# Kernel tuning notes

Measured on AMD Instinct MI355X. Metric: run time of the kernel, lower is better.

The kernel has to match this reference:

```python
import jax, jax.numpy as jnp
import numpy as np

N_NODES = 150000
N_EDGES = 300000
N_GRAPHS = 6000
HID = 256


def _lin_init(key, fan_in, fan_out):
    k1, k2 = jax.random.split(key)
    s = 1.0 / np.sqrt(fan_in)
    W = jax.random.uniform(k1, (fan_in, fan_out), jnp.float32, -s, s)
    b = jax.random.uniform(k2, (fan_out,), jnp.float32, -s, s)
    return W, b


def setup_inputs() -> dict:
    key = jax.random.key(0)
    ks = jax.random.split(key, 16)
    x = jax.random.normal(ks[0], (N_NODES, 7), jnp.float32)
    edge_index = jax.random.randint(ks[1], (2, N_EDGES), 0, N_NODES, jnp.int64)
    batch = jnp.sort(jax.random.randint(ks[2], (N_NODES,), 0, N_GRAPHS, jnp.int64))
    inp = {"x": x, "edge_index": edge_index, "batch": batch}
    dims_in = [7, HID, HID, HID]
    for i in range(4):
        Wa, ba = _lin_init(ks[3 + 2 * i], dims_in[i], HID)
        Wb, bb = _lin_init(ks[4 + 2 * i], HID, HID)
        inp[f"W{i+1}a"], inp[f"b{i+1}a"] = Wa, ba
        inp[f"W{i+1}b"], inp[f"b{i+1}b"] = Wb, bb
    inp["Wh1"], inp["bh1"] = _lin_init(ks[11], HID, 128)
    inp["Wh2"], inp["bh2"] = _lin_init(ks[12], 128, 3)
    return inp


def _gin_layer(x, src, dst, Wa, ba, Wb, bb):
    # sum-aggregate neighbor features: messages from src scattered to dst
    agg = jax.ops.segment_sum(x[src], dst, num_segments=N_NODES)
    h = agg + x  # (1 + eps) * x with eps = 0
    h = jax.nn.relu(h @ Wa + ba) @ Wb + bb  # GIN MLP
    return jax.nn.relu(h)  # outer F.relu in forward


def reference(x, edge_index, batch,
              W1a, b1a, W1b, b1b,
              W2a, b2a, W2b, b2b,
              W3a, b3a, W3b, b3b,
              W4a, b4a, W4b, b4b,
              Wh1, bh1, Wh2, bh2):
    src, dst = edge_index[0], edge_index[1]
    h = _gin_layer(x, src, dst, W1a, b1a, W1b, b1b)
    h = _gin_layer(h, src, dst, W2a, b2a, W2b, b2b)
    h = _gin_layer(h, src, dst, W3a, b3a, W3b, b3b)
    h = _gin_layer(h, src, dst, W4a, b4a, W4b, b4b)
    # global mean pool per graph
    sums = jax.ops.segment_sum(h, batch, num_segments=N_GRAPHS)
    counts = jax.ops.segment_sum(jnp.ones((N_NODES,), h.dtype), batch, num_segments=N_GRAPHS)
    pooled = sums / jnp.maximum(counts, 1.0)[:, None]
    # head (Dropout is identity in eval mode)
    out = jax.nn.relu(pooled @ Wh1 + bh1) @ Wh2 + bh2
    return out
```

## Files before the change

kernel.cpp:

```cpp
#include <hip/hip_runtime.h>

using bf16x8 = __attribute__((ext_vector_type(8))) __bf16;
using bf16x4 = __attribute__((ext_vector_type(4))) __bf16;
using f32x4  = __attribute__((ext_vector_type(4))) float;

#define MN    150000
#define NEDGE 300000
#define NG    6000
#define NSCAN 586

__device__ __forceinline__ float loadF(const void* p, size_t i, int f32) {
    return f32 ? ((const float*)p)[i] : (float)((const __bf16*)p)[i];
}
__device__ __forceinline__ int loadI(const int* p, size_t i, int i64) {
    return i64 ? p[2 * i] : p[i];
}

__global__ void k_probe(const void* W1a, const int* ei, const int* batch, int* flags) {
    __shared__ int s_f32, s_einz, s_bnz;
    if (threadIdx.x == 0) { s_f32 = 0; s_einz = 0; s_bnz = 0; }
    __syncthreads();
    const unsigned short* w = (const unsigned short*)W1a;
    for (int i = threadIdx.x; i < 1792; i += 256) {
        int e = (w[i] >> 7) & 0xFF;
        if (e >= 0xF0) s_f32 = 1;
    }
    for (int i = threadIdx.x; i < 2048; i += 256)
        if (ei[2 * i + 1] != 0) s_einz = 1;
    for (int i = threadIdx.x; i < 2048; i += 256)
        if (batch[75000 + 2 * i + 1] != 0) s_bnz = 1;
    __syncthreads();
    if (threadIdx.x == 0) {
        flags[0] = s_f32;
        flags[1] = s_einz ? 0 : 1;
        flags[2] = s_bnz ? 0 : 1;
    }
}

__global__ void k_zero_i32(int* p, int n) {
    int i = blockIdx.x * 256 + threadIdx.x;
    if (i < n) p[i] = 0;
}
__global__ void k_zero_f32(float* p, int n) {
    int i = blockIdx.x * 256 + threadIdx.x;
    if (i < n) p[i] = 0.f;
}

__global__ void k_cvtWT(const void* W0, const void* W1, const void* W2, const void* W3,
                        const void* W4, const void* W5, const void* W6,
                        __bf16* __restrict__ Wt, const int* __restrict__ flags) {
    int j = blockIdx.x >> 8;
    int n = blockIdx.x & 255, k = threadIdx.x;
    const void* Ws[7] = {W0, W1, W2, W3, W4, W5, W6};
    Wt[(size_t)j * 65536 + (size_t)n * 256 + k] = (__bf16)loadF(Ws[j], (size_t)k * 256 + n, flags[0]);
}

__global__ void k_deg(const int* __restrict__ ei, int* __restrict__ cnt, int nE,
                      const int* __restrict__ flags) {
    int e = blockIdx.x * 256 + threadIdx.x;
    if (e >= nE) return;
    int i64 = flags[1];
    int d = loadI(ei, (size_t)nE + e, i64);
    if ((unsigned)d >= (unsigned)MN) d = 0;
    atomicAdd(&cnt[d], 1);
}
__global__ void k_blksum(const int* __restrict__ cnt, int* __restrict__ bsum, int n) {
    __shared__ int s[256];
    int t = threadIdx.x;
    int i = blockIdx.x * 256 + t;
    s[t] = (i < n) ? cnt[i] : 0;
    __syncthreads();
    for (int o = 128; o > 0; o >>= 1) {
        if (t < o) s[t] += s[t + o];
        __syncthreads();
    }
    if (t == 0) bsum[blockIdx.x] = s[0];
}
__global__ __launch_bounds__(1024) void k_scanb(const int* __restrict__ bsum,
                                                int* __restrict__ bbase, int nb) {
    __shared__ int s[1024];
    int t = threadIdx.x;
    int v = (t < nb) ? bsum[t] : 0;
    s[t] = v;
    __syncthreads();
#pragma unroll
    for (int o = 1; o < 1024; o <<= 1) {
        int x = (t >= o) ? s[t - o] : 0;
        __syncthreads();
        s[t] += x;
        __syncthreads();
    }
    if (t < nb) bbase[t] = s[t] - v;
}
__global__ void k_blkscan(const int* __restrict__ cnt, const int* __restrict__ bbase,
                          int* __restrict__ offs, int n) {
    __shared__ int s[256];
    int t = threadIdx.x;
    int i = blockIdx.x * 256 + t;
    int v = (i < n) ? cnt[i] : 0;
    s[t] = v;
    __syncthreads();
    for (int o = 1; o < 256; o <<= 1) {
        int x = (t >= o) ? s[t - o] : 0;
        __syncthreads();
        s[t] += x;
        __syncthreads();
    }
    if (i < n) offs[i] = bbase[blockIdx.x] + s[t] - v;
}
__global__ void k_fill(const int* __restrict__ ei, const int* __restrict__ offs,
                       int* __restrict__ cur, int* __restrict__ elist, int nE,
                       const int* __restrict__ flags) {
    int e = blockIdx.x * 256 + threadIdx.x;
    if (e >= nE) return;
    int i64 = flags[1];
    int s = loadI(ei, (size_t)e, i64);
    int d = loadI(ei, (size_t)nE + e, i64);
    if ((unsigned)s >= (unsigned)MN) s = 0;
    if ((unsigned)d >= (unsigned)MN) d = 0;
    int pos = offs[d] + atomicAdd(&cur[d], 1);
    if ((unsigned)pos < (unsigned)NEDGE) elist[pos] = s;
}

__global__ __launch_bounds__(256) void k_l1lite(
    const void* __restrict__ x, const int* __restrict__ offs,
    const int* __restrict__ deg, const int* __restrict__ elist,
    float* __restrict__ agg7, const int* __restrict__ flags, int M_) {
    int f32 = flags[0];
    int t = threadIdx.x;
    int v = blockIdx.x * 32 + (t >> 3);
    int j = t & 7;
    if (v >= M_ || j >= 7) return;
    float s = loadF(x, (size_t)v * 7 + j, f32);
    int b = offs[v], d = min(deg[v], 1024);
    for (int e = 0; e < d; ++e) {
        int u = elist[b + e];
        if ((unsigned)u >= (unsigned)MN) u = 0;
        s += loadF(x, (size_t)u * 7 + j, f32);
    }
    agg7[(size_t)v * 8 + j] = s;
}

template<int CI, int MI>
__device__ __forceinline__ void gemm_core(const __bf16* lA, const __bf16* __restrict__ WT,
                                          int n0, int lm, int lq, f32x4 acc[CI][MI]) {
    const __bf16* wp = WT + (size_t)(n0 + lm) * 256 + lq * 8;
    bf16x8 wf[CI], wn[CI];
#pragma unroll
    for (int ci = 0; ci < CI; ++ci)
        wf[ci] = *(const bf16x8*)(wp + ci * 16 * 256);
#pragma unroll
    for (int kt = 0; kt < 8; ++kt) {
        if (kt < 7) {
#pragma unroll
            for (int ci = 0; ci < CI; ++ci)
                wn[ci] = *(const bf16x8*)(wp + ci * 16 * 256 + (kt + 1) * 32);
        }
        int sw = (((kt * 4 + lq) ^ (lm & 7)) << 3);
        bf16x8 xf[MI];
#pragma unroll
        for (int mi = 0; mi < MI; ++mi)
            xf[mi] = *(const bf16x8*)(lA + (mi * 16 + lm) * 256 + sw);
#pragma unroll
        for (int ci = 0; ci < CI; ++ci)
#pragma unroll
            for (int mi = 0; mi < MI; ++mi)
                acc[ci][mi] = __builtin_amdgcn_mfma_f32_16x16x32_bf16(
                    wf[ci], xf[mi], acc[ci][mi], 0, 0, 0);
#pragma unroll
        for (int ci = 0; ci < CI; ++ci) wf[ci] = wn[ci];
    }
}

template<int CI, int MI>
__device__ __forceinline__ void epi_to_lds(__bf16* lA, f32x4 acc[CI][MI], const void* bias,
                                           int n0, int lm, int lq, int f32) {
#pragma unroll
    for (int ci = 0; ci < CI; ++ci) {
        int n4 = n0 + ci * 16 + lq * 4;
        float b0 = loadF(bias, n4 + 0, f32), b1 = loadF(bias, n4 + 1, f32);
        float b2 = loadF(bias, n4 + 2, f32), b3 = loadF(bias, n4 + 3, f32);
#pragma unroll
        for (int mi = 0; mi < MI; ++mi) {
            int m = mi * 16 + lm;
            f32x4 a = acc[ci][mi];
            bf16x4 v;
            v[0] = (__bf16)fmaxf(a[0] + b0, 0.f);
            v[1] = (__bf16)fmaxf(a[1] + b1, 0.f);
            v[2] = (__bf16)fmaxf(a[2] + b2, 0.f);
            v[3] = (__bf16)fmaxf(a[3] + b3, 0.f);
            *(bf16x4*)(lA + m * 256 + (((n4 >> 3) ^ (m & 7)) << 3) + (n4 & 7)) = v;
        }
    }
}

template<int RW>
__device__ __forceinline__ void lds_to_global(const __bf16* lA, __bf16* __restrict__ Y,
                                              int bm, int w, int lane, int M_) {
    int half = lane >> 5;
    int cc = lane & 31;
#pragma unroll
    for (int it = 0; it < RW / 2; ++it) {
        int r = w * RW + it * 2 + half;
        int gm = bm + r;
        if (gm < M_) {
            bf16x8 v = *(const bf16x8*)(lA + r * 256 + ((cc ^ (r & 7)) << 3));
            *(bf16x8*)(Y + (size_t)gm * 256 + cc * 8) = v;
        }
    }
}

__device__ __forceinline__ void stage128_agg512(const __bf16* __restrict__ H, __bf16* lA,
                                                const int* __restrict__ offs,
                                                const int* __restrict__ deg,
                                                const int* __restrict__ elist,
                                                int bm, int t, int M_) {
    int tc = t & 7;
    int rl = t >> 3;
#pragma unroll 1
    for (int p = 0; p < 2; ++p) {
        int r = p * 64 + rl;
        int gr = bm + r;
        if (gr >= M_) gr = M_ - 1;
        const __bf16* self = H + (size_t)gr * 256 + tc * 32;
        float acc[32];
        {
            bf16x8 v0 = *(const bf16x8*)(self + 0);
            bf16x8 v1 = *(const bf16x8*)(self + 8);
            bf16x8 v2 = *(const bf16x8*)(self + 16);
            bf16x8 v3 = *(const bf16x8*)(self + 24);
#pragma unroll
            for (int j = 0; j < 8; ++j) {
                acc[j]      = (float)v0[j];
                acc[8 + j]  = (float)v1[j];
                acc[16 + j] = (float)v2[j];
                acc[24 + j] = (float)v3[j];
            }
        }
        int b = offs[gr], d = min(deg[gr], 1024);
        int e = 0;
        for (; e + 1 < d; e += 2) {
            int u0 = elist[b + e];
            int u1 = elist[b + e + 1];
            if ((unsigned)u0 >= (unsigned)MN) u0 = 0;
            if ((unsigned)u1 >= (unsigned)MN) u1 = 0;
            const __bf16* nb0 = H + (size_t)u0 * 256 + tc * 32;
            const __bf16* nb1 = H + (size_t)u1 * 256 + tc * 32;
            bf16x8 a0 = *(const bf16x8*)(nb0 + 0);
            bf16x8 a1 = *(const bf16x8*)(nb0 + 8);
            bf16x8 a2 = *(const bf16x8*)(nb0 + 16);
            bf16x8 a3 = *(const bf16x8*)(nb0 + 24);
            bf16x8 c0 = *(const bf16x8*)(nb1 + 0);
            bf16x8 c1 = *(const bf16x8*)(nb1 + 8);
            bf16x8 c2 = *(const bf16x8*)(nb1 + 16);
            bf16x8 c3 = *(const bf16x8*)(nb1 + 24);
#pragma unroll
            for (int j = 0; j < 8; ++j) {
                acc[j]      += (float)a0[j] + (float)c0[j];
                acc[8 + j]  += (float)a1[j] + (float)c1[j];
                acc[16 + j] += (float)a2[j] + (float)c2[j];
                acc[24 + j] += (float)a3[j] + (float)c3[j];
            }
        }
        if (e < d) {
            int u = elist[b + e];
            if ((unsigned)u >= (unsigned)MN) u = 0;
            const __bf16* nb = H + (size_t)u * 256 + tc * 32;
            bf16x8 n0 = *(const bf16x8*)(nb + 0);
            bf16x8 n1 = *(const bf16x8*)(nb + 8);
            bf16x8 n2 = *(const bf16x8*)(nb + 16);
            bf16x8 n3 = *(const bf16x8*)(nb + 24);
#pragma unroll
            for (int j = 0; j < 8; ++j) {
                acc[j]      += (float)n0[j];
                acc[8 + j]  += (float)n1[j];
                acc[16 + j] += (float)n2[j];
                acc[24 + j] += (float)n3[j];
            }
        }
#pragma unroll
        for (int q = 0; q < 4; ++q) {
            int c = tc * 4 + q;
            bf16x8 o;
#pragma unroll
            for (int j = 0; j < 8; ++j) o[j] = (__bf16)acc[q * 8 + j];
            *(bf16x8*)(lA + r * 256 + ((c ^ (r & 7)) << 3)) = o;
        }
    }
}

__global__ __launch_bounds__(512, 4) void k_agg_mlp(
    const __bf16* __restrict__ H, const int* __restrict__ offs, const int* __restrict__ deg,
    const int* __restrict__ elist,
    const __bf16* __restrict__ WaT, const void* __restrict__ ba,
    const __bf16* __restrict__ WbT, const void* __restrict__ bb,
    __bf16* __restrict__ Y, const int* __restrict__ batch,
    float* __restrict__ pool, float* __restrict__ cntf, int do_pool,
    int M_, const int* __restrict__ flags) {
    __shared__ __align__(16) __bf16 lA[128 * 256];
    __shared__ int sbatch[128];
    int t = threadIdx.x;
    int f32 = flags[0];
    int bm = blockIdx.x * 128;
    int w = t >> 6, lane = t & 63, lm = lane & 15, lq = lane >> 4;
    int n0 = w * 32;

    stage128_agg512(H, lA, offs, deg, elist, bm, t, M_);
    if (do_pool && t < 128) {
        int gm = bm + t;
        sbatch[t] = (gm < M_) ? loadI(batch, gm, flags[2]) : -1;
    }
    __syncthreads();

    {
        f32x4 acc[2][8] = {};
        gemm_core<2, 8>(lA, WaT, n0, lm, lq, acc);
        __syncthreads();
        epi_to_lds<2, 8>(lA, acc, ba, n0, lm, lq, f32);
    }
    __syncthreads();

    f32x4 acc2[2][8] = {};
    gemm_core<2, 8>(lA, WbT, n0, lm, lq, acc2);
    __syncthreads();
    epi_to_lds<2, 8>(lA, acc2, bb, n0, lm, lq, f32);
    __syncthreads();

    if (!do_pool) {
        lds_to_global<16>(lA, Y, bm, w, lane, M_);
    } else {
        int c = t & 255;
        int h2 = t >> 8;
        int g = -1;
        float acc = 0.f, run = 0.f;
        int rbeg = h2 * 64;
        for (int r = rbeg; r < rbeg + 64; ++r) {
            int bg = sbatch[r];
            if (bg < 0) break;
            if ((unsigned)bg >= (unsigned)NG) bg = 0;
            float v = (float)lA[r * 256 + (((c >> 3) ^ (r & 7)) << 3) + (c & 7)];
            if (bg != g) {
                if (g >= 0) {
                    atomicAdd(&pool[(size_t)g * 256 + c], acc);
                    if (c == 0) atomicAdd(&cntf[g], run);
                }
                g = bg; acc = 0.f; run = 0.f;
            }
            acc += v; run += 1.f;
        }
        if (g >= 0) {
            atomicAdd(&pool[(size_t)g * 256 + c], acc);
            if (c == 0) atomicAdd(&cntf[g], run);
        }
    }
}

__global__ __launch_bounds__(256, 2) void k_gemm1(
    const float* __restrict__ agg7, const void* __restrict__ W1a, const void* __restrict__ b1a,
    const __bf16* __restrict__ WT, const void* __restrict__ bias,
    __bf16* __restrict__ Y, int M_, const int* __restrict__ flags) {
    __shared__ __align__(16) __bf16 lA[128 * 256];
    __shared__ float sW[7 * 256];
    __shared__ float sB[256];
    int t = threadIdx.x;
    int f32 = flags[0];
    int bm = blockIdx.x * 128;
    int w = t >> 6, lane = t & 63, lm = lane & 15, lq = lane >> 4;
    int n0 = w * 64;

    sB[t] = loadF(b1a, t, f32);
#pragma unroll
    for (int k = 0; k < 7; ++k) sW[k * 256 + t] = loadF(W1a, (size_t)k * 256 + t, f32);
    __syncthreads();

    {
        int r = t >> 1;
        int gr = bm + r;
        if (gr >= M_) gr = M_ - 1;
        float a[7];
#pragma unroll
        for (int k = 0; k < 7; ++k) a[k] = agg7[(size_t)gr * 8 + k];
        int c0 = (t & 1) * 128;
#pragma unroll
        for (int s8 = 0; s8 < 16; ++s8) {
            bf16x8 o;
#pragma unroll
            for (int j = 0; j < 8; ++j) {
                int cc = c0 + s8 * 8 + j;
                float v = sB[cc];
#pragma unroll
                for (int k = 0; k < 7; ++k) v = fmaf(a[k], sW[k * 256 + cc], v);
                o[j] = (__bf16)fmaxf(v, 0.f);
            }
            int ch = (c0 >> 3) + s8;
            *(bf16x8*)(lA + r * 256 + ((ch ^ (r & 7)) << 3)) = o;
        }
    }
    __syncthreads();

    f32x4 acc[4][8] = {};
    gemm_core<4, 8>(lA, WT, n0, lm, lq, acc);
    __syncthreads();
    epi_to_lds<4, 8>(lA, acc, bias, n0, lm, lq, f32);
    __syncthreads();
    lds_to_global<32>(lA, Y, bm, w, lane, M_);
}

__global__ void k_head(const float* __restrict__ pool, const float* __restrict__ cnt,
                       const void* __restrict__ Wh1, const void* __restrict__ bh1,
                       const void* __restrict__ Wh2, const void* __restrict__ bh2,
                       void* __restrict__ outv, const int* __restrict__ flags) {
    int g = blockIdx.x, n = threadIdx.x;
    int f32 = flags[0];
    __shared__ float p[256];
    __shared__ float hid[128];
    float inv = 1.0f / fmaxf(cnt[g], 1.0f);
    for (int k = n; k < 256; k += 128) p[k] = pool[(size_t)g * 256 + k] * inv;
    __syncthreads();
    float s = loadF(bh1, n, f32);
    for (int k = 0; k < 256; ++k) s = fmaf(p[k], loadF(Wh1, (size_t)k * 128 + n, f32), s);
    hid[n] = fmaxf(s, 0.f);
    __syncthreads();
    if (n < 3) {
        float o = loadF(bh2, n, f32);
        for (int k = 0; k < 128; ++k)
            o = fmaf(hid[k], loadF(Wh2, (size_t)k * 3 + n, f32), o);
        if (f32) ((float*)outv)[(size_t)g * 3 + n] = o;
        else     ((__bf16*)outv)[(size_t)g * 3 + n] = (__bf16)o;
    }
}

extern "C" void kernel_launch(void* const* d_in, const int* in_sizes, int n_in,
                              void* d_out, int out_size, void* d_ws, size_t ws_size,
                              hipStream_t stream) {
    const void* x     = d_in[0];
    const int*  ei    = (const int*)d_in[1];
    const int*  batch = (const int*)d_in[2];
    const void *W[4][2], *b[4][2];
    for (int l = 0; l < 4; ++l) {
        W[l][0] = d_in[3 + 4 * l];
        b[l][0] = d_in[4 + 4 * l];
        W[l][1] = d_in[5 + 4 * l];
        b[l][1] = d_in[6 + 4 * l];
    }
    const void* Wh1 = d_in[19];
    const void* bh1 = d_in[20];
    const void* Wh2 = d_in[21];
    const void* bh2 = d_in[22];

    char* p = (char*)d_ws;
    auto alloc = [&](size_t bytes) -> char* {
        char* r = p;
        p += (bytes + 255) & ~(size_t)255;
        return r;
    };
    __bf16* B1    = (__bf16*)alloc((size_t)MN * 256 * 2);
    __bf16* B2    = (__bf16*)alloc((size_t)MN * 256 * 2);
    __bf16* WT    = (__bf16*)alloc((size_t)7 * 256 * 256 * 2);
    float*  AGG7  = (float*)alloc((size_t)MN * 8 * 4);
    int*    offs  = (int*)alloc((size_t)MN * 4);
    int*    cnt   = (int*)alloc((size_t)MN * 4);
    int*    elist = (int*)alloc((size_t)NEDGE * 4);
    int*    bsum  = (int*)alloc((size_t)NSCAN * 4);
    int*    bbase = (int*)alloc((size_t)NSCAN * 4);
    float*  POOL  = (float*)alloc((size_t)NG * 256 * 4);
    float*  CNTF  = (float*)alloc((size_t)NG * 4);
    int*    flags = (int*)alloc(64);

    k_probe<<<1, 256, 0, stream>>>(W[0][0], ei, batch, flags);

    k_cvtWT<<<7 * 256, 256, 0, stream>>>(W[0][1], W[1][0], W[1][1], W[2][0], W[2][1],
                                         W[3][0], W[3][1], WT, flags);

    k_zero_i32<<<NSCAN, 256, 0, stream>>>(cnt, MN);
    k_deg<<<(NEDGE + 255) / 256, 256, 0, stream>>>(ei, cnt, NEDGE, flags);
    k_blksum<<<NSCAN, 256, 0, stream>>>(cnt, bsum, MN);
    k_scanb<<<1, 1024, 0, stream>>>(bsum, bbase, NSCAN);
    k_blkscan<<<NSCAN, 256, 0, stream>>>(cnt, bbase, offs, MN);
    k_zero_i32<<<NSCAN, 256, 0, stream>>>(cnt, MN);
    k_fill<<<(NEDGE + 255) / 256, 256, 0, stream>>>(ei, offs, cnt, elist, NEDGE, flags);

    k_zero_f32<<<(NG * 257 + 255) / 256, 256, 0, stream>>>(POOL, NG * 256 + NG);

    int gblocks = (MN + 127) / 128;

    k_l1lite<<<(MN + 31) / 32, 256, 0, stream>>>(x, offs, cnt, elist, AGG7, flags, MN);
    k_gemm1<<<gblocks, 256, 0, stream>>>(AGG7, W[0][0], b[0][0], WT , b[0][1],
                                         B1, MN, flags);

    __bf16* bin = B1;
    __bf16* bout = B2;
    for (int l = 1; l < 4; ++l) {
        const __bf16* WaT = WT + (size_t)(1 + 2 * (l - 1)) * 65536;
        const __bf16* WbT = WT + (size_t)(2 + 2 * (l - 1)) * 65536;
        int dp = (l == 3) ? 1 : 0;
        k_agg_mlp<<<gblocks, 512, 0, stream>>>(bin, offs, cnt, elist,
                                               WaT, b[l][0], WbT, b[l][1], bout,
                                               batch, POOL, CNTF, dp, MN, flags);
        __bf16* tmp = bin; bin = bout; bout = tmp;
    }

    k_head<<<NG, 128, 0, stream>>>(POOL, CNTF, Wh1, bh1, Wh2, bh2, d_out, flags);
}
```

Before: 572.5 us.

## Use 256-thread agg-MLP blocks with wider per-wave GEMM tiles and row-pair gather

Switches the fused aggregate+MLP kernel from 512 to 256 threads per block. Each wave now computes 64 output columns (CI=4) instead of 32, which doubles the weight-fragment reuse per LDS A-fragment load. The neighbor gather is restructured so each half-wave handles one row with 8 contiguous bf16 per lane, processing two rows per wave at once. Weight prefetch is deepened to two k-steps ahead. The trade-off is more accumulator registers and lower thread-level parallelism per block, which may hurt latency hiding in the gather phase. The pooling loop is also serialized over all 128 rows per thread.

```diff
diff --git a/kernel.cpp b/kernel.cpp
--- a/kernel.cpp
+++ b/kernel.cpp
@@ -145,16 +145,19 @@
 __device__ __forceinline__ void gemm_core(const __bf16* lA, const __bf16* __restrict__ WT,
                                           int n0, int lm, int lq, f32x4 acc[CI][MI]) {
     const __bf16* wp = WT + (size_t)(n0 + lm) * 256 + lq * 8;
-    bf16x8 wf[CI], wn[CI];
+    bf16x8 w0[CI], w1[CI], w2[CI];
 #pragma unroll
     for (int ci = 0; ci < CI; ++ci)
-        wf[ci] = *(const bf16x8*)(wp + ci * 16 * 256);
+        w0[ci] = *(const bf16x8*)(wp + ci * 16 * 256);
+#pragma unroll
+    for (int ci = 0; ci < CI; ++ci)
+        w1[ci] = *(const bf16x8*)(wp + ci * 16 * 256 + 32);
 #pragma unroll
     for (int kt = 0; kt < 8; ++kt) {
-        if (kt < 7) {
+        if (kt < 6) {
 #pragma unroll
             for (int ci = 0; ci < CI; ++ci)
-                wn[ci] = *(const bf16x8*)(wp + ci * 16 * 256 + (kt + 1) * 32);
+                w2[ci] = *(const bf16x8*)(wp + ci * 16 * 256 + (kt + 2) * 32);
         }
         int sw = (((kt * 4 + lq) ^ (lm & 7)) << 3);
         bf16x8 xf[MI];
@@ -166,9 +169,9 @@
 #pragma unroll
             for (int mi = 0; mi < MI; ++mi)
                 acc[ci][mi] = __builtin_amdgcn_mfma_f32_16x16x32_bf16(
-                    wf[ci], xf[mi], acc[ci][mi], 0, 0, 0);
-#pragma unroll
-        for (int ci = 0; ci < CI; ++ci) wf[ci] = wn[ci];
+                    w0[ci], xf[mi], acc[ci][mi], 0, 0, 0);
+#pragma unroll
+        for (int ci = 0; ci < CI; ++ci) { w0[ci] = w1[ci]; w1[ci] = w2[ci]; }
     }
 }
 
@@ -210,86 +213,63 @@
     }
 }
 
-__device__ __forceinline__ void stage128_agg512(const __bf16* __restrict__ H, __bf16* lA,
-                                                const int* __restrict__ offs,
-                                                const int* __restrict__ deg,
-                                                const int* __restrict__ elist,
-                                                int bm, int t, int M_) {
-    int tc = t & 7;
-    int rl = t >> 3;
+__device__ __forceinline__ void stage128_pair(const __bf16* __restrict__ H, __bf16* lA,
+                                              const int* __restrict__ offs,
+                                              const int* __restrict__ deg,
+                                              const int* __restrict__ elist,
+                                              int bm, int t, int M_) {
+    int w = t >> 6, lane = t & 63;
+    int half = lane >> 5;
+    int c32 = lane & 31;
+    int cb = c32 * 8;
 #pragma unroll 1
-    for (int p = 0; p < 2; ++p) {
-        int r = p * 64 + rl;
-        int gr = bm + r;
-        if (gr >= M_) gr = M_ - 1;
-        const __bf16* self = H + (size_t)gr * 256 + tc * 32;
-        float acc[32];
-        {
-            bf16x8 v0 = *(const bf16x8*)(self + 0);
-            bf16x8 v1 = *(const bf16x8*)(self + 8);
-            bf16x8 v2 = *(const bf16x8*)(self + 16);
-            bf16x8 v3 = *(const bf16x8*)(self + 24);
-#pragma unroll
-            for (int j = 0; j < 8; ++j) {
-                acc[j]      = (float)v0[j];
-                acc[8 + j]  = (float)v1[j];
-                acc[16 + j] = (float)v2[j];
-                acc[24 + j] = (float)v3[j];
+    for (int it = 0; it < 8; ++it) {
+        int r0 = w * 32 + it * 4;
+        int myrow[2], myoff[2], mydeg[2];
+        float acc[2][8];
+#pragma unroll
+        for (int pp = 0; pp < 2; ++pp) {
+            int r = r0 + pp * 2 + half;
+            int gr = bm + r;
+            if (gr >= M_) gr = M_ - 1;
+            myrow[pp] = r;
+            myoff[pp] = offs[gr];
+            mydeg[pp] = min(deg[gr], 1024);
+            bf16x8 a = *(const bf16x8*)(H + (size_t)gr * 256 + cb);
+#pragma unroll
+            for (int j = 0; j < 8; ++j) acc[pp][j] = (float)a[j];
+        }
+        int mymax = max(mydeg[0], mydeg[1]);
+        for (int e = 0; e < mymax; ++e) {
+            bf16x8 nb[2];
+#pragma unroll
+            for (int pp = 0; pp < 2; ++pp) {
+                if (e < mydeg[pp]) {
+                    int u = elist[myoff[pp] + e];
+                    if ((unsigned)u >= (unsigned)MN) u = 0;
+                    nb[pp] = *(const bf16x8*)(H + (size_t)u * 256 + cb);
+                }
             }
-        }
-        int b = offs[gr], d = min(deg[gr], 1024);
-        int e = 0;
-        for (; e + 1 < d; e += 2) {
-            int u0 = elist[b + e];
-            int u1 = elist[b + e + 1];
-            if ((unsigned)u0 >= (unsigned)MN) u0 = 0;
-            if ((unsigned)u1 >= (unsigned)MN) u1 = 0;
-            const __bf16* nb0 = H + (size_t)u0 * 256 + tc * 32;
-            const __bf16* nb1 = H + (size_t)u1 * 256 + tc * 32;
-            bf16x8 a0 = *(const bf16x8*)(nb0 + 0);
-            bf16x8 a1 = *(const bf16x8*)(nb0 + 8);
-            bf16x8 a2 = *(const bf16x8*)(nb0 + 16);
-            bf16x8 a3 = *(const bf16x8*)(nb0 + 24);
-            bf16x8 c0 = *(const bf16x8*)(nb1 + 0);
-            bf16x8 c1 = *(const bf16x8*)(nb1 + 8);
-            bf16x8 c2 = *(const bf16x8*)(nb1 + 16);
-            bf16x8 c3 = *(const bf16x8*)(nb1 + 24);
-#pragma unroll
-            for (int j = 0; j < 8; ++j) {
-                acc[j]      += (float)a0[j] + (float)c0[j];
-                acc[8 + j]  += (float)a1[j] + (float)c1[j];
-                acc[16 + j] += (float)a2[j] + (float)c2[j];
-                acc[24 + j] += (float)a3[j] + (float)c3[j];
+#pragma unroll
+            for (int pp = 0; pp < 2; ++pp) {
+                if (e < mydeg[pp]) {
+#pragma unroll
+                    for (int j = 0; j < 8; ++j) acc[pp][j] += (float)nb[pp][j];
+                }
             }
         }
-        if (e < d) {
-            int u = elist[b + e];
-            if ((unsigned)u >= (unsigned)MN) u = 0;
-            const __bf16* nb = H + (size_t)u * 256 + tc * 32;
-            bf16x8 n0 = *(const bf16x8*)(nb + 0);
-            bf16x8 n1 = *(const bf16x8*)(nb + 8);
-            bf16x8 n2 = *(const bf16x8*)(nb + 16);
-            bf16x8 n3 = *(const bf16x8*)(nb + 24);
-#pragma unroll
-            for (int j = 0; j < 8; ++j) {
-                acc[j]      += (float)n0[j];
-                acc[8 + j]  += (float)n1[j];
-                acc[16 + j] += (float)n2[j];
-                acc[24 + j] += (float)n3[j];
-            }
-        }
-#pragma unroll
-        for (int q = 0; q < 4; ++q) {
-            int c = tc * 4 + q;
+#pragma unroll
+        for (int pp = 0; pp < 2; ++pp) {
+            int r = myrow[pp];
             bf16x8 o;
 #pragma unroll
-            for (int j = 0; j < 8; ++j) o[j] = (__bf16)acc[q * 8 + j];
-            *(bf16x8*)(lA + r * 256 + ((c ^ (r & 7)) << 3)) = o;
-        }
-    }
-}
-
-__global__ __launch_bounds__(512, 4) void k_agg_mlp(
+            for (int j = 0; j < 8; ++j) o[j] = (__bf16)acc[pp][j];
+            *(bf16x8*)(lA + r * 256 + ((c32 ^ (r & 7)) << 3)) = o;
+        }
+    }
+}
+
+__global__ __launch_bounds__(256, 2) void k_agg_mlp(
     const __bf16* __restrict__ H, const int* __restrict__ offs, const int* __restrict__ deg,
     const int* __restrict__ elist,
     const __bf16* __restrict__ WaT, const void* __restrict__ ba,
@@ -303,9 +283,9 @@
     int f32 = flags[0];
     int bm = blockIdx.x * 128;
     int w = t >> 6, lane = t & 63, lm = lane & 15, lq = lane >> 4;
-    int n0 = w * 32;
-
-    stage128_agg512(H, lA, offs, deg, elist, bm, t, M_);
+    int n0 = w * 64;
+
+    stage128_pair(H, lA, offs, deg, elist, bm, t, M_);
     if (do_pool && t < 128) {
         int gm = bm + t;
         sbatch[t] = (gm < M_) ? loadI(batch, gm, flags[2]) : -1;
@@ -313,28 +293,26 @@
     __syncthreads();
 
     {
-        f32x4 acc[2][8] = {};
-        gemm_core<2, 8>(lA, WaT, n0, lm, lq, acc);
-        __syncthreads();
-        epi_to_lds<2, 8>(lA, acc, ba, n0, lm, lq, f32);
-    }
-    __syncthreads();
-
-    f32x4 acc2[2][8] = {};
-    gemm_core<2, 8>(lA, WbT, n0, lm, lq, acc2);
-    __syncthreads();
-    epi_to_lds<2, 8>(lA, acc2, bb, n0, lm, lq, f32);
+        f32x4 acc[4][8] = {};
+        gemm_core<4, 8>(lA, WaT, n0, lm, lq, acc);
+        __syncthreads();
+        epi_to_lds<4, 8>(lA, acc, ba, n0, lm, lq, f32);
+    }
+    __syncthreads();
+
+    f32x4 acc2[4][8] = {};
+    gemm_core<4, 8>(lA, WbT, n0, lm, lq, acc2);
+    __syncthreads();
+    epi_to_lds<4, 8>(lA, acc2, bb, n0, lm, lq, f32);
     __syncthreads();
 
     if (!do_pool) {
-        lds_to_global<16>(lA, Y, bm, w, lane, M_);
+        lds_to_global<32>(lA, Y, bm, w, lane, M_);
     } else {
-        int c = t & 255;
-        int h2 = t >> 8;
+        int c = t;
         int g = -1;
         float acc = 0.f, run = 0.f;
-        int rbeg = h2 * 64;
-        for (int r = rbeg; r < rbeg + 64; ++r) {
+        for (int r = 0; r < 128; ++r) {
             int bg = sbatch[r];
             if (bg < 0) break;
             if ((unsigned)bg >= (unsigned)NG) bg = 0;
@@ -494,7 +472,7 @@
         const __bf16* WaT = WT + (size_t)(1 + 2 * (l - 1)) * 65536;
         const __bf16* WbT = WT + (size_t)(2 + 2 * (l - 1)) * 65536;
         int dp = (l == 3) ? 1 : 0;
-        k_agg_mlp<<<gblocks, 512, 0, stream>>>(bin, offs, cnt, elist,
+        k_agg_mlp<<<gblocks, 256, 0, stream>>>(bin, offs, cnt, elist,
                                                WaT, b[l][0], WbT, b[l][1], bout,
                                                batch, POOL, CNTF, dp, MN, flags);
         __bf16* tmp = bin; bin = bout; bout = tmp;
```

Measured after the change: 783.9 us. 1.37x slower.

## Sort rows by degree within each tile to balance aggregation across warps

Applied to the files above, without the earlier changes.

Adds a per-block kernel that ranks the 128 nodes of each tile by in-degree and writes a permutation. The aggregation staging then assigns rows through this permutation, so neighbouring thread groups (and thus wavefronts) handle nodes of similar degree, reducing divergence in the variable-length neighbour loop. The zero-fill kernels are also replaced with hipMemsetAsync. The cost is one extra small kernel launch and an extra indirection load per staged row.

```diff
diff --git a/kernel.cpp b/kernel.cpp
--- a/kernel.cpp
+++ b/kernel.cpp
@@ -35,15 +35,6 @@
         flags[1] = s_einz ? 0 : 1;
         flags[2] = s_bnz ? 0 : 1;
     }
-}
-
-__global__ void k_zero_i32(int* p, int n) {
-    int i = blockIdx.x * 256 + threadIdx.x;
-    if (i < n) p[i] = 0;
-}
-__global__ void k_zero_f32(float* p, int n) {
-    int i = blockIdx.x * 256 + threadIdx.x;
-    if (i < n) p[i] = 0.f;
 }
 
 __global__ void k_cvtWT(const void* W0, const void* W1, const void* W2, const void* W3,
@@ -120,6 +111,22 @@
     if ((unsigned)d >= (unsigned)MN) d = 0;
     int pos = offs[d] + atomicAdd(&cur[d], 1);
     if ((unsigned)pos < (unsigned)NEDGE) elist[pos] = s;
+}
+
+__global__ __launch_bounds__(128) void k_sortdeg(const int* __restrict__ deg,
+                                                 int* __restrict__ perm, int M_) {
+    __shared__ unsigned skey[128];
+    int b = blockIdx.x, t = threadIdx.x;
+    int gm = b * 128 + t;
+    if (gm >= M_) gm = M_ - 1;
+    int d = min(deg[gm], 255);
+    skey[t] = ((unsigned)d << 8) | (unsigned)t;
+    __syncthreads();
+    unsigned my = skey[t];
+    int rank = 0;
+#pragma unroll 8
+    for (int j = 0; j < 128; ++j) rank += (skey[j] < my) ? 1 : 0;
+    perm[b * 128 + rank] = t;
 }
 
 __global__ __launch_bounds__(256) void k_l1lite(
@@ -214,12 +221,13 @@
                                                 const int* __restrict__ offs,
                                                 const int* __restrict__ deg,
                                                 const int* __restrict__ elist,
+                                                const int* __restrict__ perm,
                                                 int bm, int t, int M_) {
     int tc = t & 7;
     int rl = t >> 3;
 #pragma unroll 1
     for (int p = 0; p < 2; ++p) {
-        int r = p * 64 + rl;
+        int r = perm[bm + p * 64 + rl];
         int gr = bm + r;
         if (gr >= M_) gr = M_ - 1;
         const __bf16* self = H + (size_t)gr * 256 + tc * 32;
@@ -291,7 +299,7 @@
 
 __global__ __launch_bounds__(512, 4) void k_agg_mlp(
     const __bf16* __restrict__ H, const int* __restrict__ offs, const int* __restrict__ deg,
-    const int* __restrict__ elist,
+    const int* __restrict__ elist, const int* __restrict__ perm,
     const __bf16* __restrict__ WaT, const void* __restrict__ ba,
     const __bf16* __restrict__ WbT, const void* __restrict__ bb,
     __bf16* __restrict__ Y, const int* __restrict__ batch,
@@ -305,7 +313,7 @@
     int w = t >> 6, lane = t & 63, lm = lane & 15, lq = lane >> 4;
     int n0 = w * 32;
 
-    stage128_agg512(H, lA, offs, deg, elist, bm, t, M_);
+    stage128_agg512(H, lA, offs, deg, elist, perm, bm, t, M_);
     if (do_pool && t < 128) {
         int gm = bm + t;
         sbatch[t] = (gm < M_) ? loadI(batch, gm, flags[2]) : -1;
@@ -454,6 +462,8 @@
         p += (bytes + 255) & ~(size_t)255;
         return r;
     };
+    int gblocks = (MN + 127) / 128;
+
     __bf16* B1    = (__bf16*)alloc((size_t)MN * 256 * 2);
     __bf16* B2    = (__bf16*)alloc((size_t)MN * 256 * 2);
     __bf16* WT    = (__bf16*)alloc((size_t)7 * 256 * 256 * 2);
@@ -463,6 +473,7 @@
     int*    elist = (int*)alloc((size_t)NEDGE * 4);
     int*    bsum  = (int*)alloc((size_t)NSCAN * 4);
     int*    bbase = (int*)alloc((size_t)NSCAN * 4);
+    int*    PERM  = (int*)alloc((size_t)gblocks * 128 * 4);
     float*  POOL  = (float*)alloc((size_t)NG * 256 * 4);
     float*  CNTF  = (float*)alloc((size_t)NG * 4);
     int*    flags = (int*)alloc(64);
@@ -472,17 +483,17 @@
     k_cvtWT<<<7 * 256, 256, 0, stream>>>(W[0][1], W[1][0], W[1][1], W[2][0], W[2][1],
                                          W[3][0], W[3][1], WT, flags);
 
-    k_zero_i32<<<NSCAN, 256, 0, stream>>>(cnt, MN);
+    hipMemsetAsync(cnt, 0, (size_t)MN * 4, stream);
     k_deg<<<(NEDGE + 255) / 256, 256, 0, stream>>>(ei, cnt, NEDGE, flags);
     k_blksum<<<NSCAN, 256, 0, stream>>>(cnt, bsum, MN);
     k_scanb<<<1, 1024, 0, stream>>>(bsum, bbase, NSCAN);
     k_blkscan<<<NSCAN, 256, 0, stream>>>(cnt, bbase, offs, MN);
-    k_zero_i32<<<NSCAN, 256, 0, stream>>>(cnt, MN);
+    hipMemsetAsync(cnt, 0, (size_t)MN * 4, stream);
     k_fill<<<(NEDGE + 255) / 256, 256, 0, stream>>>(ei, offs, cnt, elist, NEDGE, flags);
 
-    k_zero_f32<<<(NG * 257 + 255) / 256, 256, 0, stream>>>(POOL, NG * 256 + NG);
-
-    int gblocks = (MN + 127) / 128;
+    k_sortdeg<<<gblocks, 128, 0, stream>>>(cnt, PERM, MN);
+
+    hipMemsetAsync(POOL, 0, (size_t)NG * 256 * 4 + (size_t)NG * 4, stream);
 
     k_l1lite<<<(MN + 31) / 32, 256, 0, stream>>>(x, offs, cnt, elist, AGG7, flags, MN);
     k_gemm1<<<gblocks, 256, 0, stream>>>(AGG7, W[0][0], b[0][0], WT , b[0][1],
@@ -494,7 +505,7 @@
         const __bf16* WaT = WT + (size_t)(1 + 2 * (l - 1)) * 65536;
         const __bf16* WbT = WT + (size_t)(2 + 2 * (l - 1)) * 65536;
         int dp = (l == 3) ? 1 : 0;
-        k_agg_mlp<<<gblocks, 512, 0, stream>>>(bin, offs, cnt, elist,
+        k_agg_mlp<<<gblocks, 512, 0, stream>>>(bin, offs, cnt, elist, PERM,
                                                WaT, b[l][0], WbT, b[l][1], bout,
                                                batch, POOL, CNTF, dp, MN, flags);
         __bf16* tmp = bin; bin = bout; bout = tmp;
```

After: 584.9 us. 1.02x slower.

## Store first four neighbors per node inline and batch their gathers

Applied to the files above, without the earlier changes.

The fill kernel now also writes up to four source neighbors per destination node into a dense nbr4 array. The aggregation stage loads degree, offset and that int4 up front, then issues all four neighbor row gathers before accumulating, which removes the dependent elist load and raises memory-level parallelism. Nodes with more than four neighbors fall back to the elist loop. Zeroing kernels are also replaced with hipMemsetAsync; the cost is extra workspace and more registers held by the buffered loads.

```diff
diff --git a/kernel.cpp b/kernel.cpp
--- a/kernel.cpp
+++ b/kernel.cpp
@@ -35,15 +35,6 @@
         flags[1] = s_einz ? 0 : 1;
         flags[2] = s_bnz ? 0 : 1;
     }
-}
-
-__global__ void k_zero_i32(int* p, int n) {
-    int i = blockIdx.x * 256 + threadIdx.x;
-    if (i < n) p[i] = 0;
-}
-__global__ void k_zero_f32(float* p, int n) {
-    int i = blockIdx.x * 256 + threadIdx.x;
-    if (i < n) p[i] = 0.f;
 }
 
 __global__ void k_cvtWT(const void* W0, const void* W1, const void* W2, const void* W3,
@@ -109,7 +100,8 @@
     if (i < n) offs[i] = bbase[blockIdx.x] + s[t] - v;
 }
 __global__ void k_fill(const int* __restrict__ ei, const int* __restrict__ offs,
-                       int* __restrict__ cur, int* __restrict__ elist, int nE,
+                       int* __restrict__ cur, int* __restrict__ elist,
+                       int* __restrict__ nbr4, int nE,
                        const int* __restrict__ flags) {
     int e = blockIdx.x * 256 + threadIdx.x;
     if (e >= nE) return;
@@ -118,8 +110,10 @@
     int d = loadI(ei, (size_t)nE + e, i64);
     if ((unsigned)s >= (unsigned)MN) s = 0;
     if ((unsigned)d >= (unsigned)MN) d = 0;
-    int pos = offs[d] + atomicAdd(&cur[d], 1);
+    int lpos = atomicAdd(&cur[d], 1);
+    int pos = offs[d] + lpos;
     if ((unsigned)pos < (unsigned)NEDGE) elist[pos] = s;
+    if ((unsigned)lpos < 4u) nbr4[d * 4 + lpos] = s;
 }
 
 __global__ __launch_bounds__(256) void k_l1lite(
@@ -214,14 +208,25 @@
                                                 const int* __restrict__ offs,
                                                 const int* __restrict__ deg,
                                                 const int* __restrict__ elist,
+                                                const int* __restrict__ nbr4,
                                                 int bm, int t, int M_) {
     int tc = t & 7;
     int rl = t >> 3;
+    int gr_[2], b_[2], d_[2];
+    int4 e4_[2];
+#pragma unroll
+    for (int p = 0; p < 2; ++p) {
+        int gr = bm + p * 64 + rl;
+        if (gr >= M_) gr = M_ - 1;
+        gr_[p] = gr;
+        d_[p] = min(deg[gr], 1024);
+        b_[p] = offs[gr];
+        e4_[p] = *(const int4*)&nbr4[gr * 4];
+    }
 #pragma unroll 1
     for (int p = 0; p < 2; ++p) {
         int r = p * 64 + rl;
-        int gr = bm + r;
-        if (gr >= M_) gr = M_ - 1;
+        int gr = gr_[p];
         const __bf16* self = H + (size_t)gr * 256 + tc * 32;
         float acc[32];
         {
@@ -237,39 +242,42 @@
                 acc[24 + j] = (float)v3[j];
             }
         }
-        int b = offs[gr], d = min(deg[gr], 1024);
-        int e = 0;
-        for (; e + 1 < d; e += 2) {
-            int u0 = elist[b + e];
-            int u1 = elist[b + e + 1];
-            if ((unsigned)u0 >= (unsigned)MN) u0 = 0;
-            if ((unsigned)u1 >= (unsigned)MN) u1 = 0;
-            const __bf16* nb0 = H + (size_t)u0 * 256 + tc * 32;
-            const __bf16* nb1 = H + (size_t)u1 * 256 + tc * 32;
-            bf16x8 a0 = *(const bf16x8*)(nb0 + 0);
-            bf16x8 a1 = *(const bf16x8*)(nb0 + 8);
-            bf16x8 a2 = *(const bf16x8*)(nb0 + 16);
-            bf16x8 a3 = *(const bf16x8*)(nb0 + 24);
-            bf16x8 c0 = *(const bf16x8*)(nb1 + 0);
-            bf16x8 c1 = *(const bf16x8*)(nb1 + 8);
-            bf16x8 c2 = *(const bf16x8*)(nb1 + 16);
-            bf16x8 c3 = *(const bf16x8*)(nb1 + 24);
-#pragma unroll
-            for (int j = 0; j < 8; ++j) {
-                acc[j]      += (float)a0[j] + (float)c0[j];
-                acc[8 + j]  += (float)a1[j] + (float)c1[j];
-                acc[16 + j] += (float)a2[j] + (float)c2[j];
-                acc[24 + j] += (float)a3[j] + (float)c3[j];
+        int d = d_[p];
+        int u[4] = {e4_[p].x, e4_[p].y, e4_[p].z, e4_[p].w};
+#pragma unroll
+        for (int i = 0; i < 4; ++i)
+            if ((unsigned)u[i] >= (unsigned)MN) u[i] = 0;
+        bf16x8 nb[4][4];
+#pragma unroll
+        for (int i = 0; i < 4; ++i) {
+            if (i < d) {
+                const __bf16* np = H + (size_t)u[i] * 256 + tc * 32;
+                nb[i][0] = *(const bf16x8*)(np + 0);
+                nb[i][1] = *(const bf16x8*)(np + 8);
+                nb[i][2] = *(const bf16x8*)(np + 16);
+                nb[i][3] = *(const bf16x8*)(np + 24);
             }
         }
-        if (e < d) {
-            int u = elist[b + e];
-            if ((unsigned)u >= (unsigned)MN) u = 0;
-            const __bf16* nb = H + (size_t)u * 256 + tc * 32;
-            bf16x8 n0 = *(const bf16x8*)(nb + 0);
-            bf16x8 n1 = *(const bf16x8*)(nb + 8);
-            bf16x8 n2 = *(const bf16x8*)(nb + 16);
-            bf16x8 n3 = *(const bf16x8*)(nb + 24);
+#pragma unroll
+        for (int i = 0; i < 4; ++i) {
+            if (i < d) {
+#pragma unroll
+                for (int j = 0; j < 8; ++j) {
+                    acc[j]      += (float)nb[i][0][j];
+                    acc[8 + j]  += (float)nb[i][1][j];
+                    acc[16 + j] += (float)nb[i][2][j];
+                    acc[24 + j] += (float)nb[i][3][j];
+                }
+            }
+        }
+        for (int e = 4; e < d; ++e) {
+            int uu = elist[b_[p] + e];
+            if ((unsigned)uu >= (unsigned)MN) uu = 0;
+            const __bf16* np = H + (size_t)uu * 256 + tc * 32;
+            bf16x8 n0 = *(const bf16x8*)(np + 0);
+            bf16x8 n1 = *(const bf16x8*)(np + 8);
+            bf16x8 n2 = *(const bf16x8*)(np + 16);
+            bf16x8 n3 = *(const bf16x8*)(np + 24);
 #pragma unroll
             for (int j = 0; j < 8; ++j) {
                 acc[j]      += (float)n0[j];
@@ -291,7 +299,7 @@
 
 __global__ __launch_bounds__(512, 4) void k_agg_mlp(
     const __bf16* __restrict__ H, const int* __restrict__ offs, const int* __restrict__ deg,
-    const int* __restrict__ elist,
+    const int* __restrict__ elist, const int* __restrict__ nbr4,
     const __bf16* __restrict__ WaT, const void* __restrict__ ba,
     const __bf16* __restrict__ WbT, const void* __restrict__ bb,
     __bf16* __restrict__ Y, const int* __restrict__ batch,
@@ -305,7 +313,7 @@
     int w = t >> 6, lane = t & 63, lm = lane & 15, lq = lane >> 4;
     int n0 = w * 32;
 
-    stage128_agg512(H, lA, offs, deg, elist, bm, t, M_);
+    stage128_agg512(H, lA, offs, deg, elist, nbr4, bm, t, M_);
     if (do_pool && t < 128) {
         int gm = bm + t;
         sbatch[t] = (gm < M_) ? loadI(batch, gm, flags[2]) : -1;
@@ -461,6 +469,7 @@
     int*    offs  = (int*)alloc((size_t)MN * 4);
     int*    cnt   = (int*)alloc((size_t)MN * 4);
     int*    elist = (int*)alloc((size_t)NEDGE * 4);
+    int*    nbr4  = (int*)alloc((size_t)MN * 4 * 4);
     int*    bsum  = (int*)alloc((size_t)NSCAN * 4);
     int*    bbase = (int*)alloc((size_t)NSCAN * 4);
     float*  POOL  = (float*)alloc((size_t)NG * 256 * 4);
@@ -472,15 +481,15 @@
     k_cvtWT<<<7 * 256, 256, 0, stream>>>(W[0][1], W[1][0], W[1][1], W[2][0], W[2][1],
                                          W[3][0], W[3][1], WT, flags);
 
-    k_zero_i32<<<NSCAN, 256, 0, stream>>>(cnt, MN);
+    hipMemsetAsync(cnt, 0, (size_t)MN * 4, stream);
     k_deg<<<(NEDGE + 255) / 256, 256, 0, stream>>>(ei, cnt, NEDGE, flags);
     k_blksum<<<NSCAN, 256, 0, stream>>>(cnt, bsum, MN);
     k_scanb<<<1, 1024, 0, stream>>>(bsum, bbase, NSCAN);
     k_blkscan<<<NSCAN, 256, 0, stream>>>(cnt, bbase, offs, MN);
-    k_zero_i32<<<NSCAN, 256, 0, stream>>>(cnt, MN);
-    k_fill<<<(NEDGE + 255) / 256, 256, 0, stream>>>(ei, offs, cnt, elist, NEDGE, flags);
-
-    k_zero_f32<<<(NG * 257 + 255) / 256, 256, 0, stream>>>(POOL, NG * 256 + NG);
+    hipMemsetAsync(cnt, 0, (size_t)MN * 4, stream);
+    k_fill<<<(NEDGE + 255) / 256, 256, 0, stream>>>(ei, offs, cnt, elist, nbr4, NEDGE, flags);
+
+    hipMemsetAsync(POOL, 0, (size_t)NG * 256 * 4 + (size_t)NG * 4, stream);
 
     int gblocks = (MN + 127) / 128;
 
@@ -494,7 +503,7 @@
         const __bf16* WaT = WT + (size_t)(1 + 2 * (l - 1)) * 65536;
         const __bf16* WbT = WT + (size_t)(2 + 2 * (l - 1)) * 65536;
         int dp = (l == 3) ? 1 : 0;
-        k_agg_mlp<<<gblocks, 512, 0, stream>>>(bin, offs, cnt, elist,
+        k_agg_mlp<<<gblocks, 512, 0, stream>>>(bin, offs, cnt, elist, nbr4,
                                                WaT, b[l][0], WbT, b[l][1], bout,
                                                batch, POOL, CNTF, dp, MN, flags);
         __bf16* tmp = bin; bin = bout; bout = tmp;
```

After: 647.4 us. 13.1% more time.
